# Optimization experiments

Measured on AMD Instinct MI355X. Metric: run time of the kernel, lower is better.

## Reference

```python
import jax, jax.numpy as jnp
import numpy as np

N, E, C, H, L = 20000, 200000, 64, 4, 2
L0_IN, E_IN, L0_OUT = 65, 15, 64
HC = H * C
EPS = 1e-5  # InstanceNorm1d default eps
NEG_SLOPE = 0.01  # F.leaky_relu default used by DGL EGATConv


def setup_inputs() -> dict:
    key = jax.random.key(0)
    ks = jax.random.split(key, 16)
    def s(k, shape, fan):
        return (jax.random.normal(k, shape, jnp.float32) / np.float32(np.sqrt(fan)))
    return {
        "x": jax.random.normal(ks[0], (N, L0_IN), jnp.float32),
        "efeat": jax.random.normal(ks[1], (E, E_IN), jnp.float32),
        "src": jax.random.randint(ks[2], (E,), 0, N, dtype=jnp.int32),
        "dst": jax.random.randint(ks[3], (E,), 0, N, dtype=jnp.int32),
        "Wn0": s(ks[4], (L0_IN, C), L0_IN),
        "bn0": jnp.zeros((C,), jnp.float32),
        "We0": s(ks[5], (E_IN, C), E_IN),
        "be0": jnp.zeros((C,), jnp.float32),
        "Wnode": s(ks[6], (L, C, HC), C),
        "bnode": jnp.zeros((L, HC), jnp.float32),
        "Wni": s(ks[7], (L, C, HC), C),
        "Wnj": s(ks[8], (L, C, HC), C),
        "Wfij": s(ks[9], (L, C, HC), C),
        "attn": s(ks[10], (L, H, C), C),
        "bias_e": jnp.zeros((L, HC), jnp.float32),
        "Wf": s(ks[11], (C, L0_OUT), C),
        "bf": jnp.zeros((L0_OUT,), jnp.float32),
    }


def _inorm(x):
    # InstanceNorm1d on a 2D [rows, channels] tensor == per-row normalization
    m = jnp.mean(x, axis=-1, keepdims=True)
    v = jnp.var(x, axis=-1, keepdims=True)
    return (x - m) * jax.lax.rsqrt(v + EPS)


def reference(x, efeat, src, dst, Wn0, bn0, We0, be0, Wnode, bnode,
              Wni, Wnj, Wfij, attn, bias_e, Wf, bf):
    h = x @ Wn0 + bn0        # [N, C]
    f = efeat @ We0 + be0    # [E, C]
    for l in range(L):
        # edge feature update: f_out = fc_ni(h)[src] + fc_nj(h)[dst] + fc_fij(f) + bias
        f_out = (h @ Wni[l])[src] + (h @ Wnj[l])[dst] + f @ Wfij[l] + bias_e[l]  # [E, HC]
        e = jax.nn.leaky_relu(f_out, NEG_SLOPE).reshape(E, H, C)
        score = jnp.einsum('ehc,hc->eh', e, attn[l])  # [E, H]
        # edge softmax over incoming edges of each destination node
        smax = jax.ops.segment_max(score, dst, num_segments=N)
        w = jnp.exp(score - smax[dst])
        denom = jax.ops.segment_sum(w, dst, num_segments=N)
        a = w / denom[dst]                                # [E, H]
        hproj = (h @ Wnode[l] + bnode[l]).reshape(N, H, C)
        msg = hproj[src] * a[:, :, None]                  # [E, H, C]
        h_new = jax.ops.segment_sum(msg, dst, num_segments=N)  # [N, H, C]
        # mean over heads -> InstanceNorm -> ELU
        h = jax.nn.elu(_inorm(jnp.mean(h_new, axis=1)))
        f = jax.nn.elu(_inorm(jnp.mean(f_out.reshape(E, H, C), axis=1)))
    return h @ Wf + bf
```

## Files before the change

### kernel.cpp

```cpp
#include <hip/hip_runtime.h>
#include <cmath>

#define NN 20000
#define NE 200000
#define SCAN_BLOCKS 79
#define EBLK 3125
#define GRID_E 768

typedef __attribute__((ext_vector_type(8))) short bf16x8;
typedef __attribute__((ext_vector_type(4))) float f32x4;
typedef unsigned int uint;

__device__ __forceinline__ float4 ld4(const float* p){ return *(const float4*)p; }

__device__ __forceinline__ uint packbf(float a, float b) {
  uint ua = __float_as_uint(a);
  uint ub = __float_as_uint(b);
  ua = (ua + 0x7fffu + ((ua >> 16) & 1u)) >> 16;
  ub = (ub + 0x7fffu + ((ub >> 16) & 1u)) >> 16;
  return ua | (ub << 16);
}
__device__ __forceinline__ float4 up4(uint2 u) {
  return make_float4(__uint_as_float(u.x << 16), __uint_as_float(u.x & 0xffff0000u),
                     __uint_as_float(u.y << 16), __uint_as_float(u.y & 0xffff0000u));
}

__global__ void gemm16_bf16(const float* __restrict__ A, const float* __restrict__ B,
                            const float* __restrict__ bias, uint2* __restrict__ O,
                            int M, int K, const int* __restrict__ map) {
  int idx = blockIdx.x * 256 + threadIdx.x;
  if (idx >= M * 4) return;
  int m = idx >> 2, jq = idx & 3;
  const float* a = A + (long)m * K;
  const float* b = B + jq * 16;
  float c00=0,c01=0,c02=0,c03=0,c04=0,c05=0,c06=0,c07=0;
  float c08=0,c09=0,c10=0,c11=0,c12=0,c13=0,c14=0,c15=0;
  for (int k = 0; k < K; k++) {
    float av = a[k];
    const float* br = b + (long)k * 64;
    float4 b0 = ld4(br), b1 = ld4(br + 4), b2 = ld4(br + 8), b3 = ld4(br + 12);
    c00 = fmaf(av, b0.x, c00); c01 = fmaf(av, b0.y, c01); c02 = fmaf(av, b0.z, c02); c03 = fmaf(av, b0.w, c03);
    c04 = fmaf(av, b1.x, c04); c05 = fmaf(av, b1.y, c05); c06 = fmaf(av, b1.z, c06); c07 = fmaf(av, b1.w, c07);
    c08 = fmaf(av, b2.x, c08); c09 = fmaf(av, b2.y, c09); c10 = fmaf(av, b2.z, c10); c11 = fmaf(av, b2.w, c11);
    c12 = fmaf(av, b3.x, c12); c13 = fmaf(av, b3.y, c13); c14 = fmaf(av, b3.z, c14); c15 = fmaf(av, b3.w, c15);
  }
  const float* bb = bias + jq * 16;
  float4 v0 = ld4(bb), v1 = ld4(bb + 4), v2 = ld4(bb + 8), v3 = ld4(bb + 12);
  int mo = map ? map[m] : m;
  uint2* op = O + (long)mo * 16 + jq * 4;
  op[0] = make_uint2(packbf(c00 + v0.x, c01 + v0.y), packbf(c02 + v0.z, c03 + v0.w));
  op[1] = make_uint2(packbf(c04 + v1.x, c05 + v1.y), packbf(c06 + v1.z, c07 + v1.w));
  op[2] = make_uint2(packbf(c08 + v2.x, c09 + v2.y), packbf(c10 + v2.z, c11 + v2.w));
  op[3] = make_uint2(packbf(c12 + v3.x, c13 + v3.y), packbf(c14 + v3.z, c15 + v3.w));
}

__global__ void zero_i32(int* __restrict__ p, int n) {
  int i = blockIdx.x * 256 + threadIdx.x;
  if (i < n) p[i] = 0;
}

__global__ void count_deg(const int* __restrict__ dst, int* __restrict__ deg) {
  int e = blockIdx.x * 256 + threadIdx.x;
  if (e < NE) atomicAdd(&deg[dst[e]], 1);
}

__global__ void scan1(const int* __restrict__ deg, int* __restrict__ off, int* __restrict__ bsum) {
  __shared__ int buf[256];
  int t = threadIdx.x;
  int g = blockIdx.x * 256 + t;
  int v = (g < NN) ? deg[g] : 0;
  buf[t] = v;
  __syncthreads();
  for (int s = 1; s < 256; s <<= 1) {
    int x = (t >= s) ? buf[t - s] : 0;
    __syncthreads();
    buf[t] += x;
    __syncthreads();
  }
  if (g < NN) off[g] = buf[t] - v;
  if (t == 255) bsum[blockIdx.x] = buf[255];
}

__global__ void scan2(int* __restrict__ bsum, int* __restrict__ off) {
  __shared__ int buf[128];
  int t = threadIdx.x;
  int v = (t < SCAN_BLOCKS) ? bsum[t] : 0;
  buf[t] = v;
  __syncthreads();
  for (int s = 1; s < 128; s <<= 1) {
    int x = (t >= s) ? buf[t - s] : 0;
    __syncthreads();
    buf[t] += x;
    __syncthreads();
  }
  if (t < SCAN_BLOCKS) bsum[t] = buf[t] - v;
  if (t == 127) off[NN] = buf[127];
}

__global__ void scan3(int* __restrict__ off, const int* __restrict__ bsum) {
  int g = blockIdx.x * 256 + threadIdx.x;
  if (g < NN) off[g] += bsum[blockIdx.x];
}

__global__ void fill_csr(const int* __restrict__ dst, const int* __restrict__ src,
                         const int* __restrict__ off, int* __restrict__ cursor,
                         int* __restrict__ esrc, int* __restrict__ edst,
                         int* __restrict__ csr_pos) {
  int e = blockIdx.x * 256 + threadIdx.x;
  if (e >= NE) return;
  int d = dst[e];
  int p = atomicAdd(&cursor[d], 1);
  int pos = off[d] + p;
  esrc[pos] = src[e];
  edst[pos] = d;
  csr_pos[e] = pos;
}

__global__ void prep_w(const float* __restrict__ Wni, const float* __restrict__ Wnj,
                       const float* __restrict__ Wfij, const float* __restrict__ Wnode,
                       const float* __restrict__ bnode,
                       uint* __restrict__ Wcat, uint* __restrict__ WcT,
                       float* __restrict__ bmean) {
  int rid = blockIdx.x * 256 + threadIdx.x;
  if (rid < 512) {
    int l = rid >> 8, c = rid & 255;
    uint* D = Wcat + (size_t)l * 24576 + c * 96;
    for (int k8 = 0; k8 < 24; k8++) {
      int ss = k8 >> 3;
      const float* S = (ss == 0 ? Wni : ss == 1 ? Wnj : Wfij) + l * 16384;
      int kl = (k8 & 7) * 8;
      uint u0 = packbf(S[(kl+0)*256 + c], S[(kl+1)*256 + c]);
      uint u1 = packbf(S[(kl+2)*256 + c], S[(kl+3)*256 + c]);
      uint u2 = packbf(S[(kl+4)*256 + c], S[(kl+5)*256 + c]);
      uint u3 = packbf(S[(kl+6)*256 + c], S[(kl+7)*256 + c]);
      *((uint4*)(D + k8 * 4)) = make_uint4(u0, u1, u2, u3);
    }
  } else if (rid < 640) {
    int idx = rid - 512;
    int l = idx >> 6, c = idx & 63;
    const float* S = Wnode + l * 16384;
    uint* D = WcT + (size_t)l * 8192 + c * 128;
    for (int kp = 0; kp < 128; kp++) {
      int k0 = kp * 2, k1 = kp * 2 + 1;
      float v0 = S[(k0 & 63) * 256 + (k0 >> 6) * 64 + c] * 0.25f;
      float v1 = S[(k1 & 63) * 256 + (k1 >> 6) * 64 + c] * 0.25f;
      D[kp] = packbf(v0, v1);
    }
  } else if (rid < 768) {
    int idx = rid - 640;
    int l = idx >> 6, c = idx & 63;
    const float* S = bnode + l * 256;
    bmean[l * 64 + c] = 0.25f * (S[c] + S[64 + c] + S[128 + c] + S[192 + c]);
  }
}

__device__ __forceinline__ void edge_compute(
    const uint* bp, const uint* __restrict__ Wcat_l,
    const float* __restrict__ be_l, const float* __restrict__ attn_l,
    int w, int col, int quad, int ch,
    float (&ma)[2][2][4], float (&red)[4][2][33][6])
{
  bf16x8 Ba[6], Bb[6];
  Ba[0] = *(const bf16x8*)&bp[col * 36 + quad * 4];
  Ba[1] = *(const bf16x8*)&bp[col * 36 + 16 + quad * 4];
  Ba[2] = *(const bf16x8*)&bp[(32 + col) * 36 + quad * 4];
  Ba[3] = *(const bf16x8*)&bp[(32 + col) * 36 + 16 + quad * 4];
  Ba[4] = *(const bf16x8*)&bp[(64 + col) * 36 + quad * 4];
  Ba[5] = *(const bf16x8*)&bp[(64 + col) * 36 + 16 + quad * 4];
  Bb[0] = *(const bf16x8*)&bp[(16 + col) * 36 + quad * 4];
  Bb[1] = *(const bf16x8*)&bp[(16 + col) * 36 + 16 + quad * 4];
  Bb[2] = *(const bf16x8*)&bp[(48 + col) * 36 + quad * 4];
  Bb[3] = *(const bf16x8*)&bp[(48 + col) * 36 + 16 + quad * 4];
  Bb[4] = *(const bf16x8*)&bp[(80 + col) * 36 + quad * 4];
  Bb[5] = *(const bf16x8*)&bp[(80 + col) * 36 + 16 + quad * 4];
  float ma0 = 0.f, ma1 = 0.f, ma2 = 0.f, ma3 = 0.f;
  float mb0 = 0.f, mb1 = 0.f, mb2 = 0.f, mb3 = 0.f;
  float sa0 = 0.f, sa1 = 0.f, sa2 = 0.f, sa3 = 0.f;
  float sb0 = 0.f, sb1 = 0.f, sb2 = 0.f, sb3 = 0.f;
  #pragma unroll
  for (int hg = 0; hg < 4; hg++) {
    f32x4 aa = (f32x4){0.f, 0.f, 0.f, 0.f};
    f32x4 ab = (f32x4){0.f, 0.f, 0.f, 0.f};
    const uint* Ab = &Wcat_l[((4 * hg + w) * 16 + col) * 96 + quad * 4];
    #pragma unroll
    for (int kt = 0; kt < 6; kt++) {
      bf16x8 Af = *(const bf16x8*)(Ab + kt * 16);
      aa = __builtin_amdgcn_mfma_f32_16x16x32_bf16(Af, Ba[kt], aa, 0, 0, 0);
      ab = __builtin_amdgcn_mfma_f32_16x16x32_bf16(Af, Bb[kt], ab, 0, 0, 0);
    }
    int ce = (4 * hg + w) * 16 + quad * 4;
    float4 be4 = ld4(be_l + ce);
    float4 at4 = ld4(attn_l + ce);
    float xa0 = aa[0] + be4.x, xa1 = aa[1] + be4.y;
    float xa2 = aa[2] + be4.z, xa3 = aa[3] + be4.w;
    float xb0 = ab[0] + be4.x, xb1 = ab[1] + be4.y;
    float xb2 = ab[2] + be4.z, xb3 = ab[3] + be4.w;
    float la0 = xa0 > 0.f ? xa0 : 0.01f * xa0;
    float la1 = xa1 > 0.f ? xa1 : 0.01f * xa1;
    float la2 = xa2 > 0.f ? xa2 : 0.01f * xa2;
    float la3 = xa3 > 0.f ? xa3 : 0.01f * xa3;
    float lb0 = xb0 > 0.f ? xb0 : 0.01f * xb0;
    float lb1 = xb1 > 0.f ? xb1 : 0.01f * xb1;
    float lb2 = xb2 > 0.f ? xb2 : 0.01f * xb2;
    float lb3 = xb3 > 0.f ? xb3 : 0.01f * xb3;
    float dpa = la0 * at4.x + la1 * at4.y + la2 * at4.z + la3 * at4.w;
    float dpb = lb0 * at4.x + lb1 * at4.y + lb2 * at4.z + lb3 * at4.w;
    if (hg == 0) { sa0 = dpa; sb0 = dpb; }
    else if (hg == 1) { sa1 = dpa; sb1 = dpb; }
    else if (hg == 2) { sa2 = dpa; sb2 = dpb; }
    else { sa3 = dpa; sb3 = dpb; }
    ma0 += xa0; ma1 += xa1; ma2 += xa2; ma3 += xa3;
    mb0 += xb0; mb1 += xb1; mb2 += xb2; mb3 += xb3;
  }
  ma0 *= 0.25f; ma1 *= 0.25f; ma2 *= 0.25f; ma3 *= 0.25f;
  mb0 *= 0.25f; mb1 *= 0.25f; mb2 *= 0.25f; mb3 *= 0.25f;
  ma[ch][0][0] = ma0; ma[ch][0][1] = ma1; ma[ch][0][2] = ma2; ma[ch][0][3] = ma3;
  ma[ch][1][0] = mb0; ma[ch][1][1] = mb1; ma[ch][1][2] = mb2; ma[ch][1][3] = mb3;
  float s1a = ma0 + ma1 + ma2 + ma3;
  float s2a = ma0*ma0 + ma1*ma1 + ma2*ma2 + ma3*ma3;
  float s1b = mb0 + mb1 + mb2 + mb3;
  float s2b = mb0*mb0 + mb1*mb1 + mb2*mb2 + mb3*mb3;
  sa0 += __shfl_xor(sa0, 16); sa0 += __shfl_xor(sa0, 32);
  sa1 += __shfl_xor(sa1, 16); sa1 += __shfl_xor(sa1, 32);
  sa2 += __shfl_xor(sa2, 16); sa2 += __shfl_xor(sa2, 32);
  sa3 += __shfl_xor(sa3, 16); sa3 += __shfl_xor(sa3, 32);
  sb0 += __shfl_xor(sb0, 16); sb0 += __shfl_xor(sb0, 32);
  sb1 += __shfl_xor(sb1, 16); sb1 += __shfl_xor(sb1, 32);
  sb2 += __shfl_xor(sb2, 16); sb2 += __shfl_xor(sb2, 32);
  sb3 += __shfl_xor(sb3, 16); sb3 += __shfl_xor(sb3, 32);
  s1a += __shfl_xor(s1a, 16); s1a += __shfl_xor(s1a, 32);
  s2a += __shfl_xor(s2a, 16); s2a += __shfl_xor(s2a, 32);
  s1b += __shfl_xor(s1b, 16); s1b += __shfl_xor(s1b, 32);
  s2b += __shfl_xor(s2b, 16); s2b += __shfl_xor(s2b, 32);
  if (quad == 0) {
    float* ra = &red[w][ch][col][0];
    ra[0] = sa0; ra[1] = sa1; ra[2] = sa2; ra[3] = sa3; ra[4] = s1a; ra[5] = s2a;
    float* rb = &red[w][ch][16 + col][0];
    rb[0] = sb0; rb[1] = sb1; rb[2] = sb2; rb[3] = sb3; rb[4] = s1b; rb[5] = s2b;
  }
}

__global__ __launch_bounds__(256) void edge_mfma(
    const uint4* __restrict__ f_bf, const uint4* __restrict__ h_bf,
    const uint* __restrict__ Wcat_l, const float* __restrict__ be_l,
    const float* __restrict__ attn_l, const int* __restrict__ esrc,
    const int* __restrict__ edst, float* __restrict__ scc,
    uint4* __restrict__ f_next4)
{
  __shared__ uint bstage[2][96 * 36];
  __shared__ uint fout[64 * 36];
  __shared__ float red[4][2][33][6];
  int t = threadIdx.x, lane = t & 63, w = t >> 6;
  int col = lane & 15, quad = lane >> 4;
  int sr = t >> 3, sc = t & 7;
  {
    int e0 = blockIdx.x * 64 + sr;
    uint4 vs = h_bf[(long)esrc[e0] * 8 + sc];
    uint4 vd = h_bf[(long)edst[e0] * 8 + sc];
    uint4 vf = f_bf[(long)e0 * 8 + sc];
    *(uint4*)&bstage[0][sr * 36 + sc * 4] = vs;
    *(uint4*)&bstage[0][(32 + sr) * 36 + sc * 4] = vd;
    *(uint4*)&bstage[0][(64 + sr) * 36 + sc * 4] = vf;
  }
  __syncthreads();
  for (int nb = blockIdx.x; nb < EBLK; nb += GRID_E) {
    int base = nb * 64;
    int nbn = nb + GRID_E;
    float ma[2][2][4];
    int e1 = base + 32 + sr;
    uint4 p1s = h_bf[(long)esrc[e1] * 8 + sc];
    uint4 p1d = h_bf[(long)edst[e1] * 8 + sc];
    uint4 p1f = f_bf[(long)e1 * 8 + sc];
    edge_compute(&bstage[0][0], Wcat_l, be_l, attn_l, w, col, quad, 0, ma, red);
    *(uint4*)&bstage[1][sr * 36 + sc * 4] = p1s;
    *(uint4*)&bstage[1][(32 + sr) * 36 + sc * 4] = p1d;
    *(uint4*)&bstage[1][(64 + sr) * 36 + sc * 4] = p1f;
    int e2 = (nbn < EBLK ? nbn : nb) * 64 + sr;
    uint4 p0s = h_bf[(long)esrc[e2] * 8 + sc];
    uint4 p0d = h_bf[(long)edst[e2] * 8 + sc];
    uint4 p0f = f_bf[(long)e2 * 8 + sc];
    __syncthreads();
    edge_compute(&bstage[1][0], Wcat_l, be_l, attn_l, w, col, quad, 1, ma, red);
    __syncthreads();
    {
      int eL = t >> 2, hh = t & 3;
      int chx = eL >> 5, c32 = eL & 31;
      float sv = red[0][chx][c32][hh] + red[1][chx][c32][hh]
               + red[2][chx][c32][hh] + red[3][chx][c32][hh];
      scc[(long)(base + eL) * 4 + hh] = sv;
    }
    #pragma unroll
    for (int ch = 0; ch < 2; ch++) {
      #pragma unroll
      for (int sub = 0; sub < 2; sub++) {
        int c32 = sub * 16 + col;
        float s1T = red[0][ch][c32][4] + red[1][ch][c32][4]
                  + red[2][ch][c32][4] + red[3][ch][c32][4];
        float s2T = red[0][ch][c32][5] + red[1][ch][c32][5]
                  + red[2][ch][c32][5] + red[3][ch][c32][5];
        float mean = s1T * 0.015625f;
        float var  = s2T * 0.015625f - mean * mean;
        float rs = rsqrtf(var + 1e-5f);
        float o0 = (ma[ch][sub][0] - mean) * rs; o0 = o0 > 0.f ? o0 : expm1f(o0);
        float o1 = (ma[ch][sub][1] - mean) * rs; o1 = o1 > 0.f ? o1 : expm1f(o1);
        float o2 = (ma[ch][sub][2] - mean) * rs; o2 = o2 > 0.f ? o2 : expm1f(o2);
        float o3 = (ma[ch][sub][3] - mean) * rs; o3 = o3 > 0.f ? o3 : expm1f(o3);
        int eL = ch * 32 + c32;
        fout[eL * 36 + w * 8 + quad * 2]     = packbf(o0, o1);
        fout[eL * 36 + w * 8 + quad * 2 + 1] = packbf(o2, o3);
      }
    }
    *(uint4*)&bstage[0][sr * 36 + sc * 4] = p0s;
    *(uint4*)&bstage[0][(32 + sr) * 36 + sc * 4] = p0d;
    *(uint4*)&bstage[0][(64 + sr) * 36 + sc * 4] = p0f;
    __syncthreads();
    {
      int row = t >> 2, part = t & 3;
      uint4 x0 = *(uint4*)&fout[row * 36 + part * 8];
      uint4 x1 = *(uint4*)&fout[row * 36 + part * 8 + 4];
      long gp = ((long)(base + row)) * 8 + part * 2;
      f_next4[gp] = x0;
      f_next4[gp + 1] = x1;
    }
  }
}

__global__ __launch_bounds__(256) void agg_combine(
    const uint2* __restrict__ h2, const float4* __restrict__ sc_csr4,
    const int* __restrict__ esrc, const int* __restrict__ off,
    const uint4* __restrict__ WcT4, const float* __restrict__ bmean_l,
    uint4* __restrict__ h_next4)
{
  __shared__ uint gsh[16][132];
  __shared__ float red2[4][17][2];
  __shared__ uint fout2[16 * 36];
  int t = threadIdx.x, lane = t & 63, w = t >> 6;
  int col = lane & 15, quad = lane >> 4;
  int n0 = blockIdx.x * 16;
  bf16x8 A2[8];
  #pragma unroll
  for (int kt = 0; kt < 8; kt++)
    A2[kt] = *(const bf16x8*)&WcT4[(w * 16 + col) * 32 + kt * 4 + quad];
  #pragma unroll 1
  for (int nl = 0; nl < 4; nl++) {
    int n = n0 + w * 4 + nl;
    int o0 = off[n], o1 = off[n + 1];
    float mx0 = -3.0e38f, mx1 = -3.0e38f, mx2 = -3.0e38f, mx3 = -3.0e38f;
    {
      int i = o0 + quad;
      for (; i + 4 < o1; i += 8) {
        float4 sA = sc_csr4[i];
        float4 sB = sc_csr4[i + 4];
        mx0 = fmaxf(mx0, fmaxf(sA.x, sB.x)); mx1 = fmaxf(mx1, fmaxf(sA.y, sB.y));
        mx2 = fmaxf(mx2, fmaxf(sA.z, sB.z)); mx3 = fmaxf(mx3, fmaxf(sA.w, sB.w));
      }
      if (i < o1) {
        float4 s = sc_csr4[i];
        mx0 = fmaxf(mx0, s.x); mx1 = fmaxf(mx1, s.y);
        mx2 = fmaxf(mx2, s.z); mx3 = fmaxf(mx3, s.w);
      }
    }
    mx0 = fmaxf(mx0, __shfl_xor(mx0, 16)); mx0 = fmaxf(mx0, __shfl_xor(mx0, 32));
    mx1 = fmaxf(mx1, __shfl_xor(mx1, 16)); mx1 = fmaxf(mx1, __shfl_xor(mx1, 32));
    mx2 = fmaxf(mx2, __shfl_xor(mx2, 16)); mx2 = fmaxf(mx2, __shfl_xor(mx2, 32));
    mx3 = fmaxf(mx3, __shfl_xor(mx3, 16)); mx3 = fmaxf(mx3, __shfl_xor(mx3, 32));
    float d0 = 0.f, d1 = 0.f, d2 = 0.f, d3 = 0.f;
    float a00=0.f,a01=0.f,a02=0.f,a03=0.f, a10=0.f,a11=0.f,a12=0.f,a13=0.f;
    float a20=0.f,a21=0.f,a22=0.f,a23=0.f, a30=0.f,a31=0.f,a32=0.f,a33=0.f;
    #define AGG_BODY(ii) { \
      float4 s = sc_csr4[ii]; \
      int sr_ = esrc[ii]; \
      uint2 hv = h2[(long)sr_ * 16 + col]; \
      float w0 = __expf(s.x - mx0), w1 = __expf(s.y - mx1); \
      float w2 = __expf(s.z - mx2), w3 = __expf(s.w - mx3); \
      d0 += w0; d1 += w1; d2 += w2; d3 += w3; \
      float4 p = up4(hv); \
      a00 = fmaf(w0,p.x,a00); a01 = fmaf(w0,p.y,a01); a02 = fmaf(w0,p.z,a02); a03 = fmaf(w0,p.w,a03); \
      a10 = fmaf(w1,p.x,a10); a11 = fmaf(w1,p.y,a11); a12 = fmaf(w1,p.z,a12); a13 = fmaf(w1,p.w,a13); \
      a20 = fmaf(w2,p.x,a20); a21 = fmaf(w2,p.y,a21); a22 = fmaf(w2,p.z,a22); a23 = fmaf(w2,p.w,a23); \
      a30 = fmaf(w3,p.x,a30); a31 = fmaf(w3,p.y,a31); a32 = fmaf(w3,p.z,a32); a33 = fmaf(w3,p.w,a33); }
    {
      int i = o0 + quad;
      for (; i + 4 < o1; i += 8) { AGG_BODY(i); AGG_BODY(i + 4); }
      if (i < o1) { AGG_BODY(i); }
    }
    #undef AGG_BODY
    d0 += __shfl_xor(d0,16); d0 += __shfl_xor(d0,32);
    d1 += __shfl_xor(d1,16); d1 += __shfl_xor(d1,32);
    d2 += __shfl_xor(d2,16); d2 += __shfl_xor(d2,32);
    d3 += __shfl_xor(d3,16); d3 += __shfl_xor(d3,32);
    a00 += __shfl_xor(a00,16); a00 += __shfl_xor(a00,32);
    a01 += __shfl_xor(a01,16); a01 += __shfl_xor(a01,32);
    a02 += __shfl_xor(a02,16); a02 += __shfl_xor(a02,32);
    a03 += __shfl_xor(a03,16); a03 += __shfl_xor(a03,32);
    a10 += __shfl_xor(a10,16); a10 += __shfl_xor(a10,32);
    a11 += __shfl_xor(a11,16); a11 += __shfl_xor(a11,32);
    a12 += __shfl_xor(a12,16); a12 += __shfl_xor(a12,32);
    a13 += __shfl_xor(a13,16); a13 += __shfl_xor(a13,32);
    a20 += __shfl_xor(a20,16); a20 += __shfl_xor(a20,32);
    a21 += __shfl_xor(a21,16); a21 += __shfl_xor(a21,32);
    a22 += __shfl_xor(a22,16); a22 += __shfl_xor(a22,32);
    a23 += __shfl_xor(a23,16); a23 += __shfl_xor(a23,32);
    a30 += __shfl_xor(a30,16); a30 += __shfl_xor(a30,32);
    a31 += __shfl_xor(a31,16); a31 += __shfl_xor(a31,32);
    a32 += __shfl_xor(a32,16); a32 += __shfl_xor(a32,32);
    a33 += __shfl_xor(a33,16); a33 += __shfl_xor(a33,32);
    uint u0 = 0u, u1 = 0u, u2 = 0u, u3 = 0u, u4 = 0u, u5 = 0u, u6 = 0u, u7 = 0u;
    if (o0 < o1) {
      float i0 = 1.f / d0, i1 = 1.f / d1, i2 = 1.f / d2, i3 = 1.f / d3;
      u0 = packbf(a00*i0, a01*i0); u1 = packbf(a02*i0, a03*i0);
      u2 = packbf(a10*i1, a11*i1); u3 = packbf(a12*i1, a13*i1);
      u4 = packbf(a20*i2, a21*i2); u5 = packbf(a22*i2, a23*i2);
      u6 = packbf(a30*i3, a31*i3); u7 = packbf(a32*i3, a33*i3);
    }
    if (quad == 0) {
      int nloc = w * 4 + nl;
      gsh[nloc][col*2]      = u0; gsh[nloc][col*2 + 1]      = u1;
      gsh[nloc][32 + col*2] = u2; gsh[nloc][32 + col*2 + 1] = u3;
      gsh[nloc][64 + col*2] = u4; gsh[nloc][64 + col*2 + 1] = u5;
      gsh[nloc][96 + col*2] = u6; gsh[nloc][96 + col*2 + 1] = u7;
    }
  }
  __syncthreads();
  f32x4 acc = (f32x4){0.f, 0.f, 0.f, 0.f};
  #pragma unroll
  for (int kt = 0; kt < 8; kt++) {
    bf16x8 Bg = *(const bf16x8*)&gsh[col][kt * 16 + quad * 4];
    acc = __builtin_amdgcn_mfma_f32_16x16x32_bf16(A2[kt], Bg, acc, 0, 0, 0);
  }
  int n2 = n0 + col;
  int dg = off[n2 + 1] - off[n2];
  float4 bm = ld4(bmean_l + w * 16 + quad * 4);
  float x0, x1, x2, x3;
  if (dg > 0) { x0 = acc[0] + bm.x; x1 = acc[1] + bm.y; x2 = acc[2] + bm.z; x3 = acc[3] + bm.w; }
  else { x0 = x1 = x2 = x3 = 0.f; }
  float s1 = x0 + x1 + x2 + x3;
  float s2 = x0*x0 + x1*x1 + x2*x2 + x3*x3;
  s1 += __shfl_xor(s1, 16); s2 += __shfl_xor(s2, 16);
  s1 += __shfl_xor(s1, 32); s2 += __shfl_xor(s2, 32);
  if (quad == 0) { red2[w][col][0] = s1; red2[w][col][1] = s2; }
  __syncthreads();
  float s1T = red2[0][col][0] + red2[1][col][0] + red2[2][col][0] + red2[3][col][0];
  float s2T = red2[0][col][1] + red2[1][col][1] + red2[2][col][1] + red2[3][col][1];
  float mean = s1T * 0.015625f;
  float var  = s2T * 0.015625f - mean * mean;
  float rs = rsqrtf(var + 1e-5f);
  float o0 = (x0 - mean) * rs; o0 = o0 > 0.f ? o0 : expm1f(o0);
  float o1 = (x1 - mean) * rs; o1 = o1 > 0.f ? o1 : expm1f(o1);
  float o2 = (x2 - mean) * rs; o2 = o2 > 0.f ? o2 : expm1f(o2);
  float o3 = (x3 - mean) * rs; o3 = o3 > 0.f ? o3 : expm1f(o3);
  fout2[col * 36 + w * 8 + quad * 2]     = packbf(o0, o1);
  fout2[col * 36 + w * 8 + quad * 2 + 1] = packbf(o2, o3);
  __syncthreads();
  if (t < 128) {
    int row = t >> 3, part = t & 7;
    uint4 x = *(uint4*)&fout2[row * 36 + part * 4];
    h_next4[((long)(n0 + row)) * 8 + part] = x;
  }
}

__global__ void final_gemm(const uint2* __restrict__ h, const float* __restrict__ Wf,
                           const float* __restrict__ bf_, float* __restrict__ out) {
  int idx = blockIdx.x * 256 + threadIdx.x;
  if (idx >= NN * 16) return;
  int m = idx >> 4, j4 = (idx & 15) << 2;
  const uint2* row = h + (long)m * 16;
  float ax = 0.f, ay = 0.f, az = 0.f, aw = 0.f;
  for (int kk = 0; kk < 16; kk++) {
    float4 a = up4(row[kk]);
    float4 b0 = ld4(Wf + (kk * 4 + 0) * 64 + j4);
    float4 b1 = ld4(Wf + (kk * 4 + 1) * 64 + j4);
    float4 b2 = ld4(Wf + (kk * 4 + 2) * 64 + j4);
    float4 b3 = ld4(Wf + (kk * 4 + 3) * 64 + j4);
    ax = fmaf(a.x, b0.x, ax); ay = fmaf(a.x, b0.y, ay); az = fmaf(a.x, b0.z, az); aw = fmaf(a.x, b0.w, aw);
    ax = fmaf(a.y, b1.x, ax); ay = fmaf(a.y, b1.y, ay); az = fmaf(a.y, b1.z, az); aw = fmaf(a.y, b1.w, aw);
    ax = fmaf(a.z, b2.x, ax); ay = fmaf(a.z, b2.y, ay); az = fmaf(a.z, b2.z, az); aw = fmaf(a.z, b2.w, aw);
    ax = fmaf(a.w, b3.x, ax); ay = fmaf(a.w, b3.y, ay); az = fmaf(a.w, b3.z, az); aw = fmaf(a.w, b3.w, aw);
  }
  float4 bb = ld4(bf_ + j4);
  *(float4*)(out + (long)m * 64 + j4) = make_float4(ax + bb.x, ay + bb.y, az + bb.z, aw + bb.w);
}

extern "C" void kernel_launch(void* const* d_in, const int* in_sizes, int n_in,
                              void* d_out, int out_size, void* d_ws, size_t ws_size,
                              hipStream_t stream) {
  const float* x      = (const float*)d_in[0];
  const float* efeat  = (const float*)d_in[1];
  const int*   src    = (const int*)d_in[2];
  const int*   dst    = (const int*)d_in[3];
  const float* Wn0    = (const float*)d_in[4];
  const float* bn0    = (const float*)d_in[5];
  const float* We0    = (const float*)d_in[6];
  const float* be0    = (const float*)d_in[7];
  const float* Wnode  = (const float*)d_in[8];
  const float* bnode  = (const float*)d_in[9];
  const float* Wni    = (const float*)d_in[10];
  const float* Wnj    = (const float*)d_in[11];
  const float* Wfij   = (const float*)d_in[12];
  const float* attn   = (const float*)d_in[13];
  const float* bias_e = (const float*)d_in[14];
  const float* Wf     = (const float*)d_in[15];
  const float* bf     = (const float*)d_in[16];
  float* out = (float*)d_out;

  char* w = (char*)d_ws;
  auto alloc = [&](size_t nbytes) { char* p = w; w += (nbytes + 255) & ~(size_t)255; return p; };
  uint2* h_a   = (uint2*)alloc((size_t)NN * 128);
  uint2* h_b   = (uint2*)alloc((size_t)NN * 128);
  uint2* f_a   = (uint2*)alloc((size_t)NE * 128);
  uint2* f_b   = (uint2*)alloc((size_t)NE * 128);
  float* scc   = (float*)alloc((size_t)NE * 16);
  uint*  Wcat  = (uint*)alloc((size_t)2 * 24576 * 4);
  uint*  WcT   = (uint*)alloc((size_t)2 * 8192 * 4);
  float* bmean = (float*)alloc((size_t)2 * 64 * 4);
  int* deg     = (int*)alloc((size_t)NN * 2 * 4);
  int* cursor  = deg + NN;
  int* off     = (int*)alloc((size_t)(NN + 1) * 4);
  int* esrc    = (int*)alloc((size_t)NE * 4);
  int* edst    = (int*)alloc((size_t)NE * 4);
  int* csr_pos = (int*)alloc((size_t)NE * 4);
  int* bsum    = (int*)alloc((size_t)128 * 4);

  zero_i32<<<(2 * NN + 255) / 256, 256, 0, stream>>>(deg, 2 * NN);
  count_deg<<<(NE + 255) / 256, 256, 0, stream>>>(dst, deg);
  scan1<<<SCAN_BLOCKS, 256, 0, stream>>>(deg, off, bsum);
  scan2<<<1, 128, 0, stream>>>(bsum, off);
  scan3<<<SCAN_BLOCKS, 256, 0, stream>>>(off, bsum);
  fill_csr<<<(NE + 255) / 256, 256, 0, stream>>>(dst, src, off, cursor, esrc, edst, csr_pos);

  gemm16_bf16<<<(NN * 4 + 255) / 256, 256, 0, stream>>>(x, Wn0, bn0, h_a, NN, 65, nullptr);
  gemm16_bf16<<<(NE * 4 + 255) / 256, 256, 0, stream>>>(efeat, We0, be0, f_a, NE, 15, csr_pos);
  prep_w<<<4, 256, 0, stream>>>(Wni, Wnj, Wfij, Wnode, bnode, Wcat, WcT, bmean);

  uint2* hc = h_a; uint2* hn = h_b;
  uint2* fc = f_a; uint2* fn = f_b;
  for (int l = 0; l < 2; l++) {
    const uint* Wcat_l = Wcat + (size_t)l * 24576;
    const uint4* WcT_l = (const uint4*)(WcT + (size_t)l * 8192);
    const float* bm_l  = bmean + (size_t)l * 64;
    const float* be_l  = bias_e + (size_t)l * 256;
    const float* at_l  = attn + (size_t)l * 256;
    edge_mfma<<<GRID_E, 256, 0, stream>>>((const uint4*)fc, (const uint4*)hc,
                                          Wcat_l, be_l, at_l, esrc, edst, scc,
                                          (uint4*)fn);
    agg_combine<<<NN / 16, 256, 0, stream>>>((const uint2*)hc, (const float4*)scc,
                                             esrc, off, WcT_l, bm_l, (uint4*)hn);
    uint2* tmp = hc; hc = hn; hn = tmp;
    tmp = fc; fc = fn; fn = tmp;
  }
  final_gemm<<<(NN * 16 + 255) / 256, 256, 0, stream>>>(hc, Wf, bf, out);
}
```

Baseline: 421.1 us.

## Drop segment-max pass; compute exp and softmax denominators in edge kernel via atomics

The edge kernel now exponentiates attention scores directly, without subtracting a per-destination max, and atomically accumulates per-node denominators into a zeroed buffer. The aggregation kernel no longer runs the separate max pass or the exp and denominator work; it reads the precomputed weights and the denominator. This removes one pass over the CSR scores and the exp work from aggregation, at the cost of float atomics, an extra zeroing launch per layer, and overflow risk when scores are large. A small unroll pragma is also added to the initial GEMM loop.

```diff
diff --git a/kernel.cpp b/kernel.cpp
--- a/kernel.cpp
+++ b/kernel.cpp
@@ -35,6 +35,7 @@
   const float* b = B + jq * 16;
   float c00=0,c01=0,c02=0,c03=0,c04=0,c05=0,c06=0,c07=0;
   float c08=0,c09=0,c10=0,c11=0,c12=0,c13=0,c14=0,c15=0;
+  #pragma unroll 3
   for (int k = 0; k < K; k++) {
     float av = a[k];
     const float* br = b + (long)k * 64;
@@ -245,7 +246,7 @@
     const uint* __restrict__ Wcat_l, const float* __restrict__ be_l,
     const float* __restrict__ attn_l, const int* __restrict__ esrc,
     const int* __restrict__ edst, float* __restrict__ scc,
-    uint4* __restrict__ f_next4)
+    float* __restrict__ den, uint4* __restrict__ f_next4)
 {
   __shared__ uint bstage[2][96 * 36];
   __shared__ uint fout[64 * 36];
@@ -287,7 +288,9 @@
       int chx = eL >> 5, c32 = eL & 31;
       float sv = red[0][chx][c32][hh] + red[1][chx][c32][hh]
                + red[2][chx][c32][hh] + red[3][chx][c32][hh];
-      scc[(long)(base + eL) * 4 + hh] = sv;
+      float ev = __expf(sv);
+      scc[(long)(base + eL) * 4 + hh] = ev;
+      atomicAdd(&den[(long)edst[base + eL] * 4 + hh], ev);
     }
     #pragma unroll
     for (int ch = 0; ch < 2; ch++) {
@@ -328,6 +331,7 @@
 __global__ __launch_bounds__(256) void agg_combine(
     const uint2* __restrict__ h2, const float4* __restrict__ sc_csr4,
     const int* __restrict__ esrc, const int* __restrict__ off,
+    const float* __restrict__ den,
     const uint4* __restrict__ WcT4, const float* __restrict__ bmean_l,
     uint4* __restrict__ h_next4)
 {
@@ -345,50 +349,23 @@
   for (int nl = 0; nl < 4; nl++) {
     int n = n0 + w * 4 + nl;
     int o0 = off[n], o1 = off[n + 1];
-    float mx0 = -3.0e38f, mx1 = -3.0e38f, mx2 = -3.0e38f, mx3 = -3.0e38f;
-    {
-      int i = o0 + quad;
-      for (; i + 4 < o1; i += 8) {
-        float4 sA = sc_csr4[i];
-        float4 sB = sc_csr4[i + 4];
-        mx0 = fmaxf(mx0, fmaxf(sA.x, sB.x)); mx1 = fmaxf(mx1, fmaxf(sA.y, sB.y));
-        mx2 = fmaxf(mx2, fmaxf(sA.z, sB.z)); mx3 = fmaxf(mx3, fmaxf(sA.w, sB.w));
-      }
-      if (i < o1) {
-        float4 s = sc_csr4[i];
-        mx0 = fmaxf(mx0, s.x); mx1 = fmaxf(mx1, s.y);
-        mx2 = fmaxf(mx2, s.z); mx3 = fmaxf(mx3, s.w);
-      }
-    }
-    mx0 = fmaxf(mx0, __shfl_xor(mx0, 16)); mx0 = fmaxf(mx0, __shfl_xor(mx0, 32));
-    mx1 = fmaxf(mx1, __shfl_xor(mx1, 16)); mx1 = fmaxf(mx1, __shfl_xor(mx1, 32));
-    mx2 = fmaxf(mx2, __shfl_xor(mx2, 16)); mx2 = fmaxf(mx2, __shfl_xor(mx2, 32));
-    mx3 = fmaxf(mx3, __shfl_xor(mx3, 16)); mx3 = fmaxf(mx3, __shfl_xor(mx3, 32));
-    float d0 = 0.f, d1 = 0.f, d2 = 0.f, d3 = 0.f;
     float a00=0.f,a01=0.f,a02=0.f,a03=0.f, a10=0.f,a11=0.f,a12=0.f,a13=0.f;
     float a20=0.f,a21=0.f,a22=0.f,a23=0.f, a30=0.f,a31=0.f,a32=0.f,a33=0.f;
     #define AGG_BODY(ii) { \
       float4 s = sc_csr4[ii]; \
       int sr_ = esrc[ii]; \
       uint2 hv = h2[(long)sr_ * 16 + col]; \
-      float w0 = __expf(s.x - mx0), w1 = __expf(s.y - mx1); \
-      float w2 = __expf(s.z - mx2), w3 = __expf(s.w - mx3); \
-      d0 += w0; d1 += w1; d2 += w2; d3 += w3; \
       float4 p = up4(hv); \
-      a00 = fmaf(w0,p.x,a00); a01 = fmaf(w0,p.y,a01); a02 = fmaf(w0,p.z,a02); a03 = fmaf(w0,p.w,a03); \
-      a10 = fmaf(w1,p.x,a10); a11 = fmaf(w1,p.y,a11); a12 = fmaf(w1,p.z,a12); a13 = fmaf(w1,p.w,a13); \
-      a20 = fmaf(w2,p.x,a20); a21 = fmaf(w2,p.y,a21); a22 = fmaf(w2,p.z,a22); a23 = fmaf(w2,p.w,a23); \
-      a30 = fmaf(w3,p.x,a30); a31 = fmaf(w3,p.y,a31); a32 = fmaf(w3,p.z,a32); a33 = fmaf(w3,p.w,a33); }
+      a00 = fmaf(s.x,p.x,a00); a01 = fmaf(s.x,p.y,a01); a02 = fmaf(s.x,p.z,a02); a03 = fmaf(s.x,p.w,a03); \
+      a10 = fmaf(s.y,p.x,a10); a11 = fmaf(s.y,p.y,a11); a12 = fmaf(s.y,p.z,a12); a13 = fmaf(s.y,p.w,a13); \
+      a20 = fmaf(s.z,p.x,a20); a21 = fmaf(s.z,p.y,a21); a22 = fmaf(s.z,p.z,a22); a23 = fmaf(s.z,p.w,a23); \
+      a30 = fmaf(s.w,p.x,a30); a31 = fmaf(s.w,p.y,a31); a32 = fmaf(s.w,p.z,a32); a33 = fmaf(s.w,p.w,a33); }
     {
       int i = o0 + quad;
       for (; i + 4 < o1; i += 8) { AGG_BODY(i); AGG_BODY(i + 4); }
       if (i < o1) { AGG_BODY(i); }
     }
     #undef AGG_BODY
-    d0 += __shfl_xor(d0,16); d0 += __shfl_xor(d0,32);
-    d1 += __shfl_xor(d1,16); d1 += __shfl_xor(d1,32);
-    d2 += __shfl_xor(d2,16); d2 += __shfl_xor(d2,32);
-    d3 += __shfl_xor(d3,16); d3 += __shfl_xor(d3,32);
     a00 += __shfl_xor(a00,16); a00 += __shfl_xor(a00,32);
     a01 += __shfl_xor(a01,16); a01 += __shfl_xor(a01,32);
     a02 += __shfl_xor(a02,16); a02 += __shfl_xor(a02,32);
@@ -407,7 +384,8 @@
     a33 += __shfl_xor(a33,16); a33 += __shfl_xor(a33,32);
     uint u0 = 0u, u1 = 0u, u2 = 0u, u3 = 0u, u4 = 0u, u5 = 0u, u6 = 0u, u7 = 0u;
     if (o0 < o1) {
-      float i0 = 1.f / d0, i1 = 1.f / d1, i2 = 1.f / d2, i3 = 1.f / d3;
+      float4 dv = ld4(den + (long)n * 4);
+      float i0 = 1.f / dv.x, i1 = 1.f / dv.y, i2 = 1.f / dv.z, i3 = 1.f / dv.w;
       u0 = packbf(a00*i0, a01*i0); u1 = packbf(a02*i0, a03*i0);
       u2 = packbf(a10*i1, a11*i1); u3 = packbf(a12*i1, a13*i1);
       u4 = packbf(a20*i2, a21*i2); u5 = packbf(a22*i2, a23*i2);
@@ -510,6 +488,7 @@
   uint2* f_a   = (uint2*)alloc((size_t)NE * 128);
   uint2* f_b   = (uint2*)alloc((size_t)NE * 128);
   float* scc   = (float*)alloc((size_t)NE * 16);
+  float* den   = (float*)alloc((size_t)NN * 16);
   uint*  Wcat  = (uint*)alloc((size_t)2 * 24576 * 4);
   uint*  WcT   = (uint*)alloc((size_t)2 * 8192 * 4);
   float* bmean = (float*)alloc((size_t)2 * 64 * 4);
@@ -540,11 +519,12 @@
     const float* bm_l  = bmean + (size_t)l * 64;
     const float* be_l  = bias_e + (size_t)l * 256;
     const float* at_l  = attn + (size_t)l * 256;
+    zero_i32<<<(NN * 4 + 255) / 256, 256, 0, stream>>>((int*)den, NN * 4);
     edge_mfma<<<GRID_E, 256, 0, stream>>>((const uint4*)fc, (const uint4*)hc,
                                           Wcat_l, be_l, at_l, esrc, edst, scc,
-                                          (uint4*)fn);
+                                          den, (uint4*)fn);
     agg_combine<<<NN / 16, 256, 0, stream>>>((const uint2*)hc, (const float4*)scc,
-                                             esrc, off, WcT_l, bm_l, (uint4*)hn);
+                                             esrc, off, den, WcT_l, bm_l, (uint4*)hn);
     uint2* tmp = hc; hc = hn; hn = tmp;
     tmp = fc; fc = fn; fn = tmp;
   }
```

New measurement: 437.5 us. 3.9% more time.
